# Kernel optimization log

Measured on AMD Instinct MI355X. Metric: run time of the kernel, lower is better.

Reference implementation:

```python
import jax, jax.numpy as jnp
import numpy as np
import math

DIM = 1024; B = 4; S = 2048; R = 3; K = 256; MAXR = 256; H = 8; HD = DIM // H
THRESH = 0.5; EPS = 1e-5

def _gelu(x):
    return jax.nn.gelu(x, approximate=False)

def _ln(x, g, b):
    m = jnp.mean(x, axis=-1, keepdims=True)
    v = jnp.var(x, axis=-1, keepdims=True)
    return (x - m) * jax.lax.rsqrt(v + EPS) * g + b

def setup_inputs() -> dict:
    key = jax.random.key(0)
    ks = jax.random.split(key, 24)
    sd = 1.0 / math.sqrt(DIM)
    sd2 = 1.0 / math.sqrt(2 * DIM)
    return {
        'x': jax.random.normal(ks[0], (B, S, DIM), jnp.float32),
        'retrieved': jax.random.normal(ks[1], (R, B, K, DIM), jnp.float32),
        # per-retriever query generator MLPs: Linear->GELU->Linear
        'qg_w1': jax.random.normal(ks[2], (R, DIM, DIM), jnp.float32) * sd,
        'qg_b1': jnp.zeros((R, DIM), jnp.float32),
        'qg_w2': jax.random.normal(ks[3], (R, DIM, DIM), jnp.float32) * sd,
        'qg_b2': jnp.zeros((R, DIM), jnp.float32),
        # per-retriever pooler: LayerNorm -> Linear
        'pln_g': jnp.ones((R, DIM), jnp.float32),
        'pln_b': jnp.zeros((R, DIM), jnp.float32),
        'pool_w': jax.random.normal(ks[4], (R, DIM, DIM), jnp.float32) * sd,
        'pool_b': jnp.zeros((R, DIM), jnp.float32),
        # relevance scorer: Linear(2d,d/2)->GELU->Linear(d/2,1)->Sigmoid
        'rel_w1': jax.random.normal(ks[5], (2 * DIM, DIM // 2), jnp.float32) * sd2,
        'rel_b1': jnp.zeros((DIM // 2,), jnp.float32),
        'rel_w2': jax.random.normal(ks[6], (DIM // 2, 1), jnp.float32) * (1.0 / math.sqrt(DIM // 2)),
        'rel_b2': jnp.zeros((1,), jnp.float32),
        # fusion MultiheadAttention: stacked q/k/v in-proj + out-proj
        'in_w': jax.random.normal(ks[7], (3, DIM, DIM), jnp.float32) * sd,
        'in_b': jnp.zeros((3, DIM), jnp.float32),
        'out_w': jax.random.normal(ks[8], (DIM, DIM), jnp.float32) * sd,
        'out_b': jnp.zeros((DIM,), jnp.float32),
        # fusion LayerNorm
        'fln_g': jnp.ones((DIM,), jnp.float32),
        'fln_b': jnp.zeros((DIM,), jnp.float32),
    }

def reference(x, retrieved, qg_w1, qg_b1, qg_w2, qg_b2, pln_g, pln_b, pool_w, pool_b,
              rel_w1, rel_b1, rel_w2, rel_b2, in_w, in_b, out_w, out_b, fln_g, fln_b):
    # ---- query generation: per-retriever MLP + self-attn pooling ----
    qf = _gelu(jnp.einsum('bsd,rde->rbse', x, qg_w1) + qg_b1[:, None, None, :])
    qf = jnp.einsum('rbsd,rde->rbse', qf, qg_w2) + qg_b2[:, None, None, :]  # [R,B,S,D]
    attn = jax.nn.softmax(jnp.einsum('rbsd,rbtd->rbst', qf, qf) / math.sqrt(DIM), axis=-1)
    pooled = jnp.einsum('rbst,rbtd->rbsd', attn, qf).mean(axis=2)  # [R,B,D]
    pooled = _ln(pooled, pln_g[:, None, :], pln_b[:, None, :])
    queries = jnp.einsum('rbd,rde->rbe', pooled, pool_w) + pool_b[:, None, :]  # [R,B,D]
    # ---- relevance scoring of retrieved tokens against queries ----
    q_exp = jnp.broadcast_to(queries[:, :, None, :], (R, B, K, DIM))
    pairs = jnp.concatenate([retrieved, q_exp], axis=-1)  # [R,B,K,2D]
    h = _gelu(pairs @ rel_w1 + rel_b1)
    rel = jax.nn.sigmoid((h @ rel_w2 + rel_b2)[..., 0])  # [R,B,K]
    # ---- threshold mask + per-batch top-k across all retrievers ----
    cand_tok = jnp.transpose(retrieved, (1, 0, 2, 3)).reshape(B, R * K, DIM)
    cand_rel = jnp.transpose(rel, (1, 0, 2)).reshape(B, R * K)
    valid = cand_rel >= THRESH
    masked_rel = jnp.where(valid, cand_rel, -jnp.inf)
    _, top_idx = jax.lax.top_k(masked_rel, MAXR)  # [B,MAXR]
    sel_tok = jnp.take_along_axis(cand_tok, top_idx[..., None], axis=1)  # [B,MAXR,D]
    key_valid = jnp.take_along_axis(valid, top_idx, axis=1)  # [B,MAXR]
    any_valid = jnp.any(key_valid, axis=-1)  # [B]
    # ---- fusion: cross-attention x -> selected tokens, residual + LN ----
    q = (x @ in_w[0] + in_b[0]).reshape(B, S, H, HD)
    k = (sel_tok @ in_w[1] + in_b[1]).reshape(B, MAXR, H, HD)
    v = (sel_tok @ in_w[2] + in_b[2]).reshape(B, MAXR, H, HD)
    scores = jnp.einsum('bshd,bthd->bhst', q, k) / math.sqrt(HD)
    scores = jnp.where(key_valid[:, None, None, :], scores, -1e9)
    a = jax.nn.softmax(scores, axis=-1)
    fused = jnp.einsum('bhst,bthd->bshd', a, v).reshape(B, S, DIM) @ out_w + out_b
    enhanced = _ln(x + fused, fln_g, fln_b)
    return jnp.where(any_valid[:, None, None], enhanced, x)
```

## Files before the change

### kernel.cpp

```cpp
#include <hip/hip_runtime.h>
#include <math.h>


typedef unsigned short u16;
typedef unsigned int   u32;
typedef __attribute__((ext_vector_type(8))) short short8;
typedef __attribute__((ext_vector_type(4))) float f32x4;
typedef __attribute__((ext_vector_type(4))) u16  u16x4;

__device__ __forceinline__ float b2f(u16 u){ union{float f;u32 i;} x; x.i=((u32)u)<<16; return x.f; }
__device__ __forceinline__ u16 f2b(float f){ union{float f;u32 i;} x; x.f=f; u32 r=x.i+0x7fffu+((x.i>>16)&1u); return (u16)(r>>16); }
__device__ __forceinline__ float gelu_f(float v){ return 0.5f*v*(1.f+erff(v*0.70710678118654752f)); }

__device__ __forceinline__ void load_lds16(const u16* g, u16* l){
  __builtin_amdgcn_global_load_lds((const __attribute__((address_space(1))) u32*)g,
                                   (__attribute__((address_space(3))) u32*)l, 16, 0, 0);
}

__device__ __forceinline__ float waveRedSum(float v){
  #pragma unroll
  for (int o=32;o>0;o>>=1) v += __shfl_xor(v,o);
  return v;
}
__device__ __forceinline__ float waveRedMax(float v){
  #pragma unroll
  for (int o=32;o>0;o>>=1) v = fmaxf(v, __shfl_xor(v,o));
  return v;
}
__device__ float blockRedSum(float v){
  __shared__ float tmp[17];
  const int lane = threadIdx.x&63, wv = threadIdx.x>>6, nw = blockDim.x>>6;
  v = waveRedSum(v);
  __syncthreads();
  if (lane==0) tmp[wv]=v;
  __syncthreads();
  if (threadIdx.x==0){ float s=tmp[0]; for(int i=1;i<nw;i++) s+=tmp[i]; tmp[16]=s; }
  __syncthreads();
  return tmp[16];
}
__device__ float blockRedMax(float v){
  __shared__ float tmp[17];
  const int lane = threadIdx.x&63, wv = threadIdx.x>>6, nw = blockDim.x>>6;
  v = waveRedMax(v);
  __syncthreads();
  if (lane==0) tmp[wv]=v;
  __syncthreads();
  if (threadIdx.x==0){ float s=tmp[0]; for(int i=1;i<nw;i++) s=fmaxf(s,tmp[i]); tmp[16]=s; }
  __syncthreads();
  return tmp[16];
}

enum { EPI_NONE=0, EPI_BIAS=1, EPI_SCALE=3, EPI_VT=5 };

template<int EPI>
__global__ __launch_bounds__(512,4)
void gemm_nt(const u16* __restrict__ Ag, long long lda, long long sA1, long long sA2,
             const u16* __restrict__ Bg, long long ldb, long long sB1, long long sB2,
             u16* __restrict__ Cg, long long ldc, long long sC1, long long sC2,
             const float* __restrict__ bias, long long sBias,
             float scale, int K, int H)
{
  __shared__ u16 As[2*4096];
  __shared__ u16 Bs[2*4096];
  const int z  = blockIdx.z;
  const int zb = z / H, zh = z - zb*H;
  const u16* A = Ag + zb*sA1 + zh*sA2;
  const u16* B = Bg + zb*sB1 + zh*sB2;
  const int m0 = blockIdx.y*128, n0 = blockIdx.x*128;
  const int t  = threadIdx.x;
  const int lane = t & 63, wv = t >> 6;
  const int wm = (wv>>1)*32, wn = (wv&1)*64;

  const u16* ga0 = A + (long long)(m0 + (t>>2))*lda + (t&3)*8;
  const u16* gb0 = B + (long long)(n0 + (t>>2))*ldb + (t&3)*8;
  u16* lA0 = As + t*8;
  u16* lB0 = Bs + t*8;

  f32x4 acc[2][4];
  #pragma unroll
  for (int i=0;i<2;i++)
    #pragma unroll
    for (int j=0;j<4;j++) acc[i][j] = (f32x4){0.f,0.f,0.f,0.f};

  const short8* arp = (const short8*)(As + (wm + (lane&15))*32 + ((lane>>4)*8));
  const short8* brp = (const short8*)(Bs + (wn + (lane&15))*32 + ((lane>>4)*8));

  #define STAGE_NT(bo) do{ \
    load_lds16(ga0, lA0+(bo)); \
    load_lds16(gb0, lB0+(bo)); \
    ga0 += 32; gb0 += 32; }while(0)

  const int nk = K >> 5;
  STAGE_NT(0);
  asm volatile("s_waitcnt vmcnt(0)" ::: "memory");
  __builtin_amdgcn_s_barrier();
  int cur = 0;
  for (int kk = 0; kk < nk; ++kk) {
    if (kk+1 < nk) STAGE_NT((cur^1)*4096);
    const int boS = cur*512;
    short8 af[2], bfr[4];
    #pragma unroll
    for (int i=0;i<2;i++) af[i]  = arp[boS + i*64];
    #pragma unroll
    for (int j=0;j<4;j++) bfr[j] = brp[boS + j*64];
    #pragma unroll
    for (int i=0;i<2;i++)
      #pragma unroll
      for (int j=0;j<4;j++)
        acc[i][j] = __builtin_amdgcn_mfma_f32_16x16x32_bf16(af[i], bfr[j], acc[i][j], 0, 0, 0);
    asm volatile("s_waitcnt vmcnt(0)" ::: "memory");
    __builtin_amdgcn_s_barrier();
    cur ^= 1;
  }
  #undef STAGE_NT

  u16* C = Cg + zb*sC1 + zh*sC2;
  const float* bz = bias + zb*sBias;
  const int rb0 = m0 + wm + ((lane>>4)<<2);
  const int cb0 = n0 + wn + (lane&15);
  #pragma unroll
  for (int j=0;j<4;j++){
    const int cn = cb0 + j*16;
    float bv = 0.f;
    if constexpr (EPI==EPI_BIAS || EPI==EPI_VT) bv = bz[cn];
    #pragma unroll
    for (int i=0;i<2;i++){
      #pragma unroll
      for (int p=0;p<4;p++){
        const int row = rb0 + i*16 + p;
        float v = acc[i][j][p];
        if constexpr (EPI==EPI_SCALE) v *= scale;
        if constexpr (EPI==EPI_BIAS)  v += bv;
        if constexpr (EPI==EPI_VT) {
          v += bv;
          const int bb = row>>8, tt = row&255, hh = cn>>7, dd = cn&127;
          C[((long long)((bb*8+hh)*128+dd)<<8) + tt] = f2b(v);
        } else {
          C[(long long)row*ldc + cn] = f2b(v);
        }
      }
    }
  }
}

enum { SP_GELU_SPLIT=0, SP_BIAS_SPLIT=1, SP_SCALE_F32=2, SP_QBG_F32=3 };

template<int EPI>
__global__ __launch_bounds__(512,4)
void gemm_nt_split(const u16* __restrict__ Ah_, const u16* __restrict__ Al_, long long lda, long long sAz,
                   const u16* __restrict__ Bh_, const u16* __restrict__ Bl_, long long ldb, long long sBz,
                   void* __restrict__ C0, void* __restrict__ C1, long long ldc, long long sCz,
                   const float* __restrict__ bias, float scale, int K)
{
  __shared__ u16 AsH[2*4096];
  __shared__ u16 AsL[2*4096];
  __shared__ u16 BsH[2*4096];
  __shared__ u16 BsL[2*4096];
  const int z = blockIdx.z;
  const int m0 = blockIdx.y*128, n0 = blockIdx.x*128;
  const int t  = threadIdx.x;
  const int lane = t & 63, wv = t >> 6;
  const int wm = (wv>>1)*32, wn = (wv&1)*64;

  const long long arow = (long long)z*sAz + (long long)(m0 + (t>>2))*lda + (t&3)*8;
  const long long brow = (long long)z*sBz + (long long)(n0 + (t>>2))*ldb + (t&3)*8;
  const u16* gah0 = Ah_ + arow;
  const u16* gal0 = Al_ + arow;
  const u16* gbh0 = Bh_ + brow;
  const u16* gbl0 = Bl_ + brow;
  u16* lAh0 = AsH + t*8;  u16* lAl0 = AsL + t*8;
  u16* lBh0 = BsH + t*8;  u16* lBl0 = BsL + t*8;

  f32x4 acc[2][4];
  #pragma unroll
  for (int i=0;i<2;i++)
    #pragma unroll
    for (int j=0;j<4;j++) acc[i][j] = (f32x4){0.f,0.f,0.f,0.f};

  const int foff = (lane&15)*32 + ((lane>>4)*8);
  const short8* arh = (const short8*)(AsH + wm*32 + foff);
  const short8* arl = (const short8*)(AsL + wm*32 + foff);
  const short8* brh = (const short8*)(BsH + wn*32 + foff);
  const short8* brl = (const short8*)(BsL + wn*32 + foff);

  #define STAGE_SP(bo) do{ \
    load_lds16(gah0, lAh0+(bo)); load_lds16(gal0, lAl0+(bo)); \
    load_lds16(gbh0, lBh0+(bo)); load_lds16(gbl0, lBl0+(bo)); \
    gah0 += 32; gal0 += 32; gbh0 += 32; gbl0 += 32; }while(0)

  const int nk = K >> 5;
  STAGE_SP(0);
  asm volatile("s_waitcnt vmcnt(0)" ::: "memory");
  __builtin_amdgcn_s_barrier();
  int cur = 0;
  for (int kk = 0; kk < nk; ++kk) {
    if (kk+1 < nk) STAGE_SP((cur^1)*4096);
    const int boS = cur*512;
    short8 fah[2], fal[2], fbh[4], fbl[4];
    #pragma unroll
    for (int i=0;i<2;i++){ fah[i]=arh[boS+i*64]; fal[i]=arl[boS+i*64]; }
    #pragma unroll
    for (int j=0;j<4;j++){ fbh[j]=brh[boS+j*64]; fbl[j]=brl[boS+j*64]; }
    #pragma unroll
    for (int i=0;i<2;i++)
      #pragma unroll
      for (int j=0;j<4;j++){
        acc[i][j] = __builtin_amdgcn_mfma_f32_16x16x32_bf16(fal[i], fbh[j], acc[i][j], 0, 0, 0);
        acc[i][j] = __builtin_amdgcn_mfma_f32_16x16x32_bf16(fah[i], fbl[j], acc[i][j], 0, 0, 0);
        acc[i][j] = __builtin_amdgcn_mfma_f32_16x16x32_bf16(fah[i], fbh[j], acc[i][j], 0, 0, 0);
      }
    asm volatile("s_waitcnt vmcnt(0)" ::: "memory");
    __builtin_amdgcn_s_barrier();
    cur ^= 1;
  }
  #undef STAGE_SP

  const int rb0 = m0 + wm + ((lane>>4)<<2);
  const int cb0 = n0 + wn + (lane&15);
  #pragma unroll
  for (int j=0;j<4;j++){
    const int cn = cb0 + j*16;
    float bv = 0.f;
    if constexpr (EPI==SP_GELU_SPLIT || EPI==SP_BIAS_SPLIT) bv = bias[cn];
    #pragma unroll
    for (int i=0;i<2;i++){
      #pragma unroll
      for (int p=0;p<4;p++){
        const int row = rb0 + i*16 + p;
        float v = acc[i][j][p];
        const long long o = (long long)z*sCz + (long long)row*ldc + cn;
        if constexpr (EPI==SP_GELU_SPLIT || EPI==SP_BIAS_SPLIT){
          v += bv;
          if constexpr (EPI==SP_GELU_SPLIT) v = gelu_f(v);
          const u16 h = f2b(v);
          ((u16*)C0)[o] = h;
          ((u16*)C1)[o] = f2b(v - b2f(h));
        }
        if constexpr (EPI==SP_SCALE_F32) ((float*)C0)[o] = v*scale;
        if constexpr (EPI==SP_QBG_F32)   ((float*)C0)[o] = gelu_f(v + bias[(row>>8)*512 + cn]);
      }
    }
  }
}

__global__ void transpose_w(const float* __restrict__ in, u16* __restrict__ out, int rows, int cols){
  __shared__ float tl[32][33];
  const long long zo = (long long)blockIdx.z*rows*cols;
  const int c0 = blockIdx.x*32, r0 = blockIdx.y*32;
  const int tx = threadIdx.x, ty = threadIdx.y;
  #pragma unroll
  for (int yy=ty; yy<32; yy+=8) tl[yy][tx] = in[zo + (long long)(r0+yy)*cols + (c0+tx)];
  __syncthreads();
  #pragma unroll
  for (int yy=ty; yy<32; yy+=8) out[zo + (long long)(c0+yy)*rows + (r0+tx)] = f2b(tl[tx][yy]);
}

__global__ void split_transpose_w(const float* __restrict__ in, u16* __restrict__ outH,
                                  u16* __restrict__ outL, int rows, int cols){
  __shared__ float tl[32][33];
  const long long zo = (long long)blockIdx.z*rows*cols;
  const int c0 = blockIdx.x*32, r0 = blockIdx.y*32;
  const int tx = threadIdx.x, ty = threadIdx.y;
  #pragma unroll
  for (int yy=ty; yy<32; yy+=8) tl[yy][tx] = in[zo + (long long)(r0+yy)*cols + (c0+tx)];
  __syncthreads();
  #pragma unroll
  for (int yy=ty; yy<32; yy+=8){
    const float v = tl[tx][yy];
    const u16 h = f2b(v);
    const long long o = zo + (long long)(c0+yy)*rows + (r0+tx);
    outH[o] = h;
    outL[o] = f2b(v - b2f(h));
  }
}

__global__ void split_f32_k(const float* __restrict__ in, u16* __restrict__ oh,
                            u16* __restrict__ ol, int n4){
  const int i = blockIdx.x*256 + threadIdx.x;
  if (i < n4){
    const float4 v = ((const float4*)in)[i];
    u16x4 hh, ll;
    hh.x=f2b(v.x); ll.x=f2b(v.x-b2f(hh.x));
    hh.y=f2b(v.y); ll.y=f2b(v.y-b2f(hh.y));
    hh.z=f2b(v.z); ll.z=f2b(v.z-b2f(hh.z));
    hh.w=f2b(v.w); ll.w=f2b(v.w-b2f(hh.w));
    ((u16x4*)oh)[i] = hh;
    ((u16x4*)ol)[i] = ll;
  }
}

__global__ void zero_f32(float* __restrict__ p, int n){
  const int i = blockIdx.x*256 + threadIdx.x;
  if (i < n) p[i] = 0.f;
}

__global__ void init_queries(const float* __restrict__ pb, float* __restrict__ q){
  const int i = blockIdx.x*256 + threadIdx.x;
  if (i < 12288) q[i] = pb[(i>>12)*1024 + (i&1023)];
}
__global__ void init_qpart(const float* __restrict__ rb1, float* __restrict__ qp){
  const int i = blockIdx.x*256 + threadIdx.x;
  if (i < 6144) qp[i] = rb1[i&511];
}

__global__ void ws_report(float* __restrict__ out, int n4, float val){
  const int i = blockIdx.x*256 + threadIdx.x;
  if (i < n4){
    float4 z; z.x = (i==0)? val : 0.f; z.y=0.f; z.z=0.f; z.w=0.f;
    ((float4*)out)[i] = z;
  }
}

__global__ void row_stats_f32(const float* __restrict__ S, float* __restrict__ mOut,
                              float* __restrict__ dOut){
  const int row = blockIdx.x;
  const float4* p = (const float4*)(S + (long long)row*2048);
  const int tid = threadIdx.x;
  const float4 a = p[2*tid], b = p[2*tid+1];
  float v[8] = {a.x,a.y,a.z,a.w,b.x,b.y,b.z,b.w};
  float mx = v[0];
  #pragma unroll
  for (int k=1;k<8;k++) mx = fmaxf(mx, v[k]);
  mx = blockRedMax(mx);
  float s = 0.f;
  #pragma unroll
  for (int k=0;k<8;k++) s += expf(v[k]-mx);
  s = blockRedSum(s);
  if (tid==0){ mOut[row]=mx; dOut[row]=s; }
}

__global__ void col_mean_f32(const float* __restrict__ S, const float* __restrict__ m,
                             const float* __restrict__ den, float* __restrict__ w){
  const int tc = blockIdx.x*256 + threadIdx.x;
  const int s0 = blockIdx.y*64;
  const float* p = S + (long long)s0*2048 + tc;
  float acc = 0.f;
  for (int s=0;s<64;s++)
    acc += expf(p[(long long)s<<11] - m[s0+s]) * (1.0f/den[s0+s]);
  atomicAdd(&w[tc], acc * (1.f/2048.f));
}

__global__ __launch_bounds__(256)
void pooled_par(const u16* __restrict__ qfh, const u16* __restrict__ qfl,
                const float* __restrict__ w, float* __restrict__ pooled){
  const int b = blockIdx.x, tt0 = blockIdx.y*128;
  const int t = threadIdx.x;
  __shared__ float wsh[128];
  if (t < 128) wsh[t] = w[b*2048 + tt0 + t];
  __syncthreads();
  const long long base = (long long)b*2097152 + (long long)tt0*1024;
  const u16* ph = qfh + base;
  const u16* pl = qfl + base;
  float acc[4] = {0.f,0.f,0.f,0.f};
  for (int s=0; s<128; s++){
    const float wt = wsh[s];
    const long long o = (long long)s*1024;
    #pragma unroll
    for (int k=0;k<4;k++){
      const int dd = t + k*256;
      acc[k] += wt*(b2f(ph[o+dd]) + b2f(pl[o+dd]));
    }
  }
  #pragma unroll
  for (int k=0;k<4;k++) atomicAdd(&pooled[b*1024 + t + k*256], acc[k]);
}

__global__ __launch_bounds__(1024)
void pool_ln(const float* __restrict__ pooled, const float* __restrict__ pg,
             const float* __restrict__ pb, float* __restrict__ plbuf){
  const int z = blockIdx.x, r = z>>2, d = threadIdx.x;
  const float v = pooled[z*1024+d];
  const float mean = blockRedSum(v) * (1.f/1024.f);
  const float df = v - mean;
  const float var = blockRedSum(df*df) * (1.f/1024.f);
  plbuf[z*1024+d] = df*rsqrtf(var+1e-5f)*pg[r*1024+d] + pb[r*1024+d];
}

__global__ __launch_bounds__(256)
void query_accum(const float* __restrict__ plbuf, const float* __restrict__ pw,
                 float* __restrict__ queries){
  const int z = blockIdx.x, r = z>>2, k0 = blockIdx.y*32;
  const int t = threadIdx.x;
  __shared__ float pls[32];
  if (t < 32) pls[t] = plbuf[z*1024 + k0 + t];
  __syncthreads();
  const float* wp = pw + (long long)r*1048576 + (long long)k0*1024;
  float acc[4] = {0.f,0.f,0.f,0.f};
  for (int s=0;s<32;s++){
    const float wv = pls[s];
    #pragma unroll
    for (int c=0;c<4;c++) acc[c] += wv*wp[s*1024 + t + c*256];
  }
  #pragma unroll
  for (int c=0;c<4;c++) atomicAdd(&queries[z*1024 + t + c*256], acc[c]);
}

__global__ __launch_bounds__(256)
void qpart_accum(const float* __restrict__ queries, const float* __restrict__ rw1,
                 float* __restrict__ qpart){
  const int z = blockIdx.x, k0 = blockIdx.y*64;
  const int t = threadIdx.x;
  __shared__ float qs[64];
  if (t < 64) qs[t] = queries[z*1024 + k0 + t];
  __syncthreads();
  const float* wp = rw1 + 1024*512 + (long long)k0*512;
  float acc[2] = {0.f,0.f};
  for (int s=0;s<64;s++){
    const float wv = qs[s];
    #pragma unroll
    for (int c=0;c<2;c++) acc[c] += wv*wp[s*512 + t + c*256];
  }
  #pragma unroll
  for (int c=0;c<2;c++) atomicAdd(&qpart[z*512 + t + c*256], acc[c]);
}

__global__ void rel_score_f32(const float* __restrict__ h, const float* __restrict__ w2,
                              const float* __restrict__ b2p, float* __restrict__ relv){
  const int row = blockIdx.x*4 + (threadIdx.x>>6);
  const int lane = threadIdx.x & 63;
  const float* p = h + (long long)row*512;
  float a = 0.f;
  #pragma unroll
  for (int k=0;k<8;k++){ const int idx = lane + k*64; a += p[idx]*w2[idx]; }
  a = waveRedSum(a);
  if (lane==0){
    const float lg = a + b2p[0];
    relv[row] = 1.f/(1.f+expf(-lg));
  }
}

__global__ __launch_bounds__(768)
void select_topk(const float* __restrict__ relv, int* __restrict__ selidx,
                 int* __restrict__ neff, int* __restrict__ anyv){
  const int b = blockIdx.x, c = threadIdx.x;
  __shared__ float rv[768];
  __shared__ int cnt;
  rv[c] = relv[(((c>>8)*4)+b)*256 + (c&255)];
  if (c==0) cnt = 0;
  __syncthreads();
  const float mine = rv[c];
  const bool valid = (mine >= 0.5f);
  int rank = 0;
  for (int j=0;j<768;j++){
    const float vj = rv[j];
    if (vj >= 0.5f && (vj > mine || (vj == mine && j < c))) rank++;
  }
  if (valid && rank < 256){
    const int s = atomicAdd(&cnt, 1);
    selidx[b*256 + s] = c;
  }
  __syncthreads();
  if (c==0){ neff[b] = cnt; anyv[b] = (cnt>0) ? 1 : 0; }
}

__global__ void gather_sel(const u16* __restrict__ rb16, const int* __restrict__ selidx,
                           const int* __restrict__ neff, u16* __restrict__ seltok){
  const int slot = blockIdx.x, b = blockIdx.y, tid = threadIdx.x;
  uint2 val; val.x=0u; val.y=0u;
  if (slot < neff[b]){
    const int c = selidx[b*256+slot];
    const uint2* src = (const uint2*)(rb16 + (long long)(((c>>8)*4+b)*256 + (c&255))*1024);
    val = src[tid];
  }
  ((uint2*)(seltok + (long long)(b*256+slot)*1024))[tid] = val;
}

__global__ void attn_softmax(u16* __restrict__ S, const int* __restrict__ neff){
  const int ri = blockIdx.x*4 + (threadIdx.x>>6);
  const int lane = threadIdx.x & 63;
  const int b = ri >> 14;
  const int ne = neff[b];
  u16* p = S + (long long)ri*256 + lane*4;
  if (ne == 0){ uint2 zz; zz.x=0u; zz.y=0u; *(uint2*)p = zz; return; }
  uint2 raw = *(const uint2*)p;
  u16 uu[4] = {(u16)(raw.x&0xffffu),(u16)(raw.x>>16),(u16)(raw.y&0xffffu),(u16)(raw.y>>16)};
  float xs[4];
  #pragma unroll
  for (int q2=0;q2<4;q2++){ const int tt = lane*4+q2; xs[q2] = (tt<ne)? b2f(uu[q2]) : -1e30f; }
  float mx = fmaxf(fmaxf(xs[0],xs[1]),fmaxf(xs[2],xs[3]));
  mx = waveRedMax(mx);
  float e[4]; float sm=0.f;
  #pragma unroll
  for (int q2=0;q2<4;q2++){ e[q2] = (lane*4+q2<ne)? expf(xs[q2]-mx) : 0.f; sm += e[q2]; }
  sm = waveRedSum(sm);
  const float inv = 1.f/sm;
  #pragma unroll
  for (int q2=0;q2<4;q2++) uu[q2] = f2b(e[q2]*inv);
  raw.x = (u32)uu[0] | ((u32)uu[1]<<16);
  raw.y = (u32)uu[2] | ((u32)uu[3]<<16);
  *(uint2*)p = raw;
}

__global__ void final_ln(const float* __restrict__ x, const u16* __restrict__ fused,
                         const float* __restrict__ g, const float* __restrict__ bb,
                         const int* __restrict__ anyv, float* __restrict__ out){
  const int row = blockIdx.x; const int b = row>>11; const int tid = threadIdx.x;
  const float4 xv = ((const float4*)(x + (long long)row*1024))[tid];
  const uint2 fv = ((const uint2*)(fused + (long long)row*1024))[tid];
  const float e0 = xv.x + b2f((u16)(fv.x&0xffffu));
  const float e1 = xv.y + b2f((u16)(fv.x>>16));
  const float e2 = xv.z + b2f((u16)(fv.y&0xffffu));
  const float e3 = xv.w + b2f((u16)(fv.y>>16));
  const float mean = blockRedSum(e0+e1+e2+e3) * (1.f/1024.f);
  const float d0=e0-mean, d1=e1-mean, d2=e2-mean, d3=e3-mean;
  const float var = blockRedSum(d0*d0+d1*d1+d2*d2+d3*d3) * (1.f/1024.f);
  const float inv = rsqrtf(var + 1e-5f);
  const float4 gv = ((const float4*)g)[tid];
  const float4 bv = ((const float4*)bb)[tid];
  float4 o;
  if (anyv[b]){
    o.x = d0*inv*gv.x + bv.x; o.y = d1*inv*gv.y + bv.y;
    o.z = d2*inv*gv.z + bv.z; o.w = d3*inv*gv.w + bv.w;
  } else o = xv;
  ((float4*)(out + (long long)row*1024))[tid] = o;
}

extern "C" void kernel_launch(void* const* d_in, const int* in_sizes, int n_in,
                              void* d_out, int out_size, void* d_ws, size_t ws_size,
                              hipStream_t stream) {
  (void)in_sizes; (void)n_in;
  const float* x      = (const float*)d_in[0];
  const float* retr   = (const float*)d_in[1];
  const float* qg_w1  = (const float*)d_in[2];
  const float* qg_b1  = (const float*)d_in[3];
  const float* qg_w2  = (const float*)d_in[4];
  const float* qg_b2  = (const float*)d_in[5];
  const float* pln_g  = (const float*)d_in[6];
  const float* pln_b  = (const float*)d_in[7];
  const float* pool_w = (const float*)d_in[8];
  const float* pool_b = (const float*)d_in[9];
  const float* rel_w1 = (const float*)d_in[10];
  const float* rel_b1 = (const float*)d_in[11];
  const float* rel_w2 = (const float*)d_in[12];
  const float* rel_b2 = (const float*)d_in[13];
  const float* in_w   = (const float*)d_in[14];
  const float* in_b   = (const float*)d_in[15];
  const float* out_w  = (const float*)d_in[16];
  const float* out_b  = (const float*)d_in[17];
  const float* fln_g  = (const float*)d_in[18];
  const float* fln_b  = (const float*)d_in[19];
  float* out = (float*)d_out;
  char* ws = (char*)d_ws;

  const size_t MB = 1u<<20;
  const size_t REQUIRED = 131*MB;
  if (ws_size < REQUIRED){
    ws_report<<<(out_size/4 + 255)/256, 256, 0, stream>>>(out, out_size/4, (float)(ws_size>>20));
    return;
  }

  u16* qg1Th = (u16*)(ws + 0*MB);
  u16* qg1Tl = (u16*)(ws + 6*MB);
  u16* qg2Th = (u16*)(ws + 12*MB);
  u16* qg2Tl = (u16*)(ws + 18*MB);
  u16* xh    = (u16*)(ws + 24*MB);
  u16* xl    = (u16*)(ws + 40*MB);
  u16* qfh   = (u16*)(ws + 56*MB);
  u16* qfl   = (u16*)(ws + 72*MB);
  u16* t1h   = (u16*)(ws + 88*MB);
  u16* t1l   = (u16*)(ws + 104*MB);
  float* scoresA = (float*)(ws + 88*MB);
  float* scoresB = (float*)(ws + 104*MB);
  u16* rh    = (u16*)(ws + 0*MB);
  u16* rl    = (u16*)(ws + 6*MB);
  u16* relTh = (u16*)(ws + 12*MB);
  u16* relTl = (u16*)(ws + 13*MB);
  u16* seltok= (u16*)(ws + 14*MB);
  u16* kbuf  = (u16*)(ws + 16*MB);
  u16* VT    = (u16*)(ws + 18*MB);
  float* hbuf= (float*)(ws + 88*MB);
  u16* inT   = (u16*)(ws + 40*MB);
  u16* outT  = (u16*)(ws + 46*MB);
  u16* qbuf  = (u16*)(ws + 56*MB);
  u16* fused = (u16*)(ws + 72*MB);
  u16* Sattn = (u16*)(ws + 88*MB);
  u16* attnout=(u16*)(ws + 0*MB);
  char* SM = ws + 120*MB;
  float* wbuf    = (float*)(SM);
  float* pooledB = (float*)(SM + 98304);
  float* plbuf   = (float*)(SM + 147456);
  float* queries = (float*)(SM + 196608);
  float* qpart   = (float*)(SM + 245760);
  float* relv    = (float*)(SM + 270336);
  int*   selidx  = (int*)(SM + 282624);
  int*   neff    = (int*)(SM + 286720);
  int*   anyv    = (int*)(SM + 286784);
  float* mrow0   = (float*)(SM + 286848);
  float* drow0   = (float*)(SM + 295040);
  float* mrow1   = (float*)(SM + 303232);
  float* drow1   = (float*)(SM + 311424);

  dim3 b256(256);
  dim3 b512(512);
  dim3 tb(32,8);
  const long long SCZ = (long long)(16*MB)/4;

  split_transpose_w<<<dim3(32,32,3), tb, 0, stream>>>(qg_w1, qg1Th, qg1Tl, 1024, 1024);
  split_transpose_w<<<dim3(32,32,3), tb, 0, stream>>>(qg_w2, qg2Th, qg2Tl, 1024, 1024);
  split_f32_k<<<8192, b256, 0, stream>>>(x, xh, xl, 2097152);
  zero_f32<<<144, b256, 0, stream>>>(wbuf, 36864);

  for (int r = 0; r < 3; r++){
    const long long wo = (long long)r*1048576;
    gemm_nt_split<SP_GELU_SPLIT><<<dim3(8,64,1), b512, 0, stream>>>(
        xh, xl, 1024, 0,  qg1Th+wo, qg1Tl+wo, 1024, 0,
        t1h, t1l, 1024, 0,  qg_b1+r*1024, 1.f, 1024);
    gemm_nt_split<SP_BIAS_SPLIT><<<dim3(8,64,1), b512, 0, stream>>>(
        t1h, t1l, 1024, 0,  qg2Th+wo, qg2Tl+wo, 1024, 0,
        qfh, qfl, 1024, 0,  qg_b2+r*1024, 1.f, 1024);
    for (int p2 = 0; p2 < 2; p2++){
      const long long qo = (long long)(p2*2)*2097152;
      gemm_nt_split<SP_SCALE_F32><<<dim3(16,16,2), b512, 0, stream>>>(
          qfh+qo, qfl+qo, 1024, 2097152,  qfh+qo, qfl+qo, 1024, 2097152,
          scoresA, nullptr, 2048, SCZ,  nullptr, 0.03125f, 1024);
      row_stats_f32<<<2048, b256, 0, stream>>>(scoresA, mrow0, drow0);
      row_stats_f32<<<2048, b256, 0, stream>>>(scoresB, mrow1, drow1);
      col_mean_f32<<<dim3(8,32), b256, 0, stream>>>(scoresA, mrow0, drow0, wbuf + (r*4+p2*2  )*2048);
      col_mean_f32<<<dim3(8,32), b256, 0, stream>>>(scoresB, mrow1, drow1, wbuf + (r*4+p2*2+1)*2048);
    }
    pooled_par<<<dim3(4,16), b256, 0, stream>>>(qfh, qfl, wbuf + r*8192, pooledB + r*4096);
  }
  pool_ln<<<12, 1024, 0, stream>>>(pooledB, pln_g, pln_b, plbuf);
  init_queries<<<48, b256, 0, stream>>>(pool_b, queries);
  query_accum<<<dim3(12,32), b256, 0, stream>>>(plbuf, pool_w, queries);

  split_f32_k<<<3072, b256, 0, stream>>>(retr, rh, rl, 786432);
  split_transpose_w<<<dim3(16,32,1), tb, 0, stream>>>(rel_w1, relTh, relTl, 1024, 512);
  init_qpart<<<24, b256, 0, stream>>>(rel_b1, qpart);
  qpart_accum<<<dim3(12,16), b256, 0, stream>>>(queries, rel_w1, qpart);
  gemm_nt_split<SP_QBG_F32><<<dim3(4,24,1), b512, 0, stream>>>(
      rh, rl, 1024, 0,  relTh, relTl, 1024, 0,  hbuf, nullptr, 512, 0,  qpart, 1.f, 1024);
  rel_score_f32<<<768, b256, 0, stream>>>(hbuf, rel_w2, rel_b2, relv);

  select_topk<<<4, 768, 0, stream>>>(relv, selidx, neff, anyv);
  gather_sel<<<dim3(256,4), b256, 0, stream>>>(rh, selidx, neff, seltok);

  transpose_w<<<dim3(32,32,3), tb, 0, stream>>>(in_w,  inT,  1024, 1024);
  transpose_w<<<dim3(32,32,1), tb, 0, stream>>>(out_w, outT, 1024, 1024);
  gemm_nt<EPI_BIAS><<<dim3(8,64,1), b512, 0, stream>>>(
      xh,1024,0,0,  inT,1024,0,0,  qbuf,1024,0,0,  in_b,0, 1.f, 1024, 1);
  gemm_nt<EPI_BIAS><<<dim3(8,8,1), b512, 0, stream>>>(
      seltok,1024,0,0,  inT+1048576,1024,0,0,  kbuf,1024,0,0,  in_b+1024,0, 1.f, 1024, 1);
  gemm_nt<EPI_VT><<<dim3(8,8,1), b512, 0, stream>>>(
      seltok,1024,0,0,  inT+2097152,1024,0,0,  VT,0,0,0,  in_b+2048,0, 1.f, 1024, 1);
  gemm_nt<EPI_SCALE><<<dim3(2,16,32), b512, 0, stream>>>(
      qbuf,1024,2097152,128,  kbuf,1024,262144,128,  Sattn,256,4194304,524288,
      (const float*)nullptr,0, 0.08838834764831845f, 128, 8);
  attn_softmax<<<16384, b256, 0, stream>>>(Sattn, neff);
  gemm_nt<EPI_NONE><<<dim3(1,16,32), b512, 0, stream>>>(
      Sattn,256,4194304,524288,  VT,256,262144,32768,  attnout,1024,2097152,128,
      (const float*)nullptr,0, 1.f, 256, 8);
  gemm_nt<EPI_BIAS><<<dim3(8,64,1), b512, 0, stream>>>(
      attnout,1024,0,0,  outT,1024,0,0,  fused,1024,0,0,  out_b,0, 1.f, 1024, 1);
  final_ln<<<8192, b256, 0, stream>>>(x, fused, fln_g, fln_b, anyv, out);
}
```

Baseline: 1.396 ms.

## Fuse softmax row statistics into score GEMM epilogue and merge column-mean launches

The self-attention score GEMM now computes per-tile partial row max and sum-of-exp in its epilogue using shuffles across the 16 lanes sharing a row. A small merge kernel combines the 32 partials per row into the final max and denominator. This replaces two full reads of the 2048x2048 fp32 score matrices by the row_stats kernels. The two col_mean launches are also folded into one launch with a z dimension. The cost is extra epilogue work and shuffles in the GEMM, plus more register pressure in it.

Measured after the change: 1.297 ms. 7.1% less time.

```diff
diff --git a/kernel.cpp b/kernel.cpp
--- a/kernel.cpp
+++ b/kernel.cpp
@@ -143,14 +143,15 @@
   }
 }
 
-enum { SP_GELU_SPLIT=0, SP_BIAS_SPLIT=1, SP_SCALE_F32=2, SP_QBG_F32=3 };
+enum { SP_GELU_SPLIT=0, SP_BIAS_SPLIT=1, SP_SCALE_F32=2, SP_QBG_F32=3, SP_SCALE_STATS=4 };
 
 template<int EPI>
 __global__ __launch_bounds__(512,4)
 void gemm_nt_split(const u16* __restrict__ Ah_, const u16* __restrict__ Al_, long long lda, long long sAz,
                    const u16* __restrict__ Bh_, const u16* __restrict__ Bl_, long long ldb, long long sBz,
                    void* __restrict__ C0, void* __restrict__ C1, long long ldc, long long sCz,
-                   const float* __restrict__ bias, float scale, int K)
+                   const float* __restrict__ bias, float scale, int K,
+                   float* __restrict__ pm, float* __restrict__ ps)
 {
   __shared__ u16 AsH[2*4096];
   __shared__ u16 AsL[2*4096];
@@ -236,10 +237,56 @@
           ((u16*)C0)[o] = h;
           ((u16*)C1)[o] = f2b(v - b2f(h));
         }
-        if constexpr (EPI==SP_SCALE_F32) ((float*)C0)[o] = v*scale;
+        if constexpr (EPI==SP_SCALE_F32 || EPI==SP_SCALE_STATS) ((float*)C0)[o] = v*scale;
         if constexpr (EPI==SP_QBG_F32)   ((float*)C0)[o] = gelu_f(v + bias[(row>>8)*512 + cn]);
       }
     }
+  }
+
+  if constexpr (EPI==SP_SCALE_STATS){
+    const int g = blockIdx.x*2 + (wv&1);
+    #pragma unroll
+    for (int i=0;i<2;i++){
+      #pragma unroll
+      for (int p=0;p<4;p++){
+        float mx = -3.4e38f;
+        #pragma unroll
+        for (int j=0;j<4;j++) mx = fmaxf(mx, acc[i][j][p]*scale);
+        #pragma unroll
+        for (int o=1;o<16;o<<=1) mx = fmaxf(mx, __shfl_xor(mx,o));
+        float sm = 0.f;
+        #pragma unroll
+        for (int j=0;j<4;j++) sm += expf(acc[i][j][p]*scale - mx);
+        #pragma unroll
+        for (int o=1;o<16;o<<=1) sm += __shfl_xor(sm,o);
+        if ((lane&15)==0){
+          const int row = rb0 + i*16 + p;
+          const long long pi = ((long long)z*2048 + row)*32 + g;
+          pm[pi] = mx; ps[pi] = sm;
+        }
+      }
+    }
+  }
+}
+
+__global__ __launch_bounds__(256)
+void merge_stats(const float* __restrict__ pm, const float* __restrict__ ps,
+                 float* __restrict__ m0o, float* __restrict__ d0o,
+                 float* __restrict__ m1o, float* __restrict__ d1o){
+  const int wv = threadIdx.x>>6, lane = threadIdx.x&63;
+  const int row = blockIdx.x*8 + wv*2 + (lane>>5);
+  const int g = lane & 31;
+  const long long pi = (long long)row*32 + g;
+  const float mg = pm[pi];
+  float m = mg;
+  #pragma unroll
+  for (int o=1;o<32;o<<=1) m = fmaxf(m, __shfl_xor(m,o));
+  float s = ps[pi] * expf(mg - m);
+  #pragma unroll
+  for (int o=1;o<32;o<<=1) s += __shfl_xor(s,o);
+  if (g==0){
+    if (row < 2048){ m0o[row]=m; d0o[row]=s; }
+    else           { m1o[row-2048]=m; d1o[row-2048]=s; }
   }
 }
 
@@ -311,33 +358,20 @@
   }
 }
 
-__global__ void row_stats_f32(const float* __restrict__ S, float* __restrict__ mOut,
-                              float* __restrict__ dOut){
-  const int row = blockIdx.x;
-  const float4* p = (const float4*)(S + (long long)row*2048);
-  const int tid = threadIdx.x;
-  const float4 a = p[2*tid], b = p[2*tid+1];
-  float v[8] = {a.x,a.y,a.z,a.w,b.x,b.y,b.z,b.w};
-  float mx = v[0];
-  #pragma unroll
-  for (int k=1;k<8;k++) mx = fmaxf(mx, v[k]);
-  mx = blockRedMax(mx);
-  float s = 0.f;
-  #pragma unroll
-  for (int k=0;k<8;k++) s += expf(v[k]-mx);
-  s = blockRedSum(s);
-  if (tid==0){ mOut[row]=mx; dOut[row]=s; }
-}
-
-__global__ void col_mean_f32(const float* __restrict__ S, const float* __restrict__ m,
-                             const float* __restrict__ den, float* __restrict__ w){
+__global__ void col_mean2(const float* __restrict__ S, long long sz,
+                          const float* __restrict__ m0a, const float* __restrict__ den0,
+                          const float* __restrict__ m1a, const float* __restrict__ den1,
+                          float* __restrict__ w){
+  const int zz = blockIdx.z;
+  const float* m   = zz ? m1a : m0a;
+  const float* den = zz ? den1 : den0;
   const int tc = blockIdx.x*256 + threadIdx.x;
   const int s0 = blockIdx.y*64;
-  const float* p = S + (long long)s0*2048 + tc;
+  const float* p = S + (long long)zz*sz + (long long)s0*2048 + tc;
   float acc = 0.f;
   for (int s=0;s<64;s++)
     acc += expf(p[(long long)s<<11] - m[s0+s]) * (1.0f/den[s0+s]);
-  atomicAdd(&w[tc], acc * (1.f/2048.f));
+  atomicAdd(&w[zz*2048 + tc], acc * (1.f/2048.f));
 }
 
 __global__ __launch_bounds__(256)
@@ -589,6 +623,8 @@
   float* drow0   = (float*)(SM + 295040);
   float* mrow1   = (float*)(SM + 303232);
   float* drow1   = (float*)(SM + 311424);
+  float* partM   = (float*)(SM + 512*1024);
+  float* partS   = (float*)(SM + 1536*1024);
 
   dim3 b256(256);
   dim3 b512(512);
@@ -604,19 +640,18 @@
     const long long wo = (long long)r*1048576;
     gemm_nt_split<SP_GELU_SPLIT><<<dim3(8,64,1), b512, 0, stream>>>(
         xh, xl, 1024, 0,  qg1Th+wo, qg1Tl+wo, 1024, 0,
-        t1h, t1l, 1024, 0,  qg_b1+r*1024, 1.f, 1024);
+        t1h, t1l, 1024, 0,  qg_b1+r*1024, 1.f, 1024, nullptr, nullptr);
     gemm_nt_split<SP_BIAS_SPLIT><<<dim3(8,64,1), b512, 0, stream>>>(
         t1h, t1l, 1024, 0,  qg2Th+wo, qg2Tl+wo, 1024, 0,
-        qfh, qfl, 1024, 0,  qg_b2+r*1024, 1.f, 1024);
+        qfh, qfl, 1024, 0,  qg_b2+r*1024, 1.f, 1024, nullptr, nullptr);
     for (int p2 = 0; p2 < 2; p2++){
       const long long qo = (long long)(p2*2)*2097152;
-      gemm_nt_split<SP_SCALE_F32><<<dim3(16,16,2), b512, 0, stream>>>(
+      gemm_nt_split<SP_SCALE_STATS><<<dim3(16,16,2), b512, 0, stream>>>(
           qfh+qo, qfl+qo, 1024, 2097152,  qfh+qo, qfl+qo, 1024, 2097152,
-          scoresA, nullptr, 2048, SCZ,  nullptr, 0.03125f, 1024);
-      row_stats_f32<<<2048, b256, 0, stream>>>(scoresA, mrow0, drow0);
-      row_stats_f32<<<2048, b256, 0, stream>>>(scoresB, mrow1, drow1);
-      col_mean_f32<<<dim3(8,32), b256, 0, stream>>>(scoresA, mrow0, drow0, wbuf + (r*4+p2*2  )*2048);
-      col_mean_f32<<<dim3(8,32), b256, 0, stream>>>(scoresB, mrow1, drow1, wbuf + (r*4+p2*2+1)*2048);
+          scoresA, nullptr, 2048, SCZ,  nullptr, 0.03125f, 1024, partM, partS);
+      merge_stats<<<512, b256, 0, stream>>>(partM, partS, mrow0, drow0, mrow1, drow1);
+      col_mean2<<<dim3(8,32,2), b256, 0, stream>>>(
+          scoresA, SCZ, mrow0, drow0, mrow1, drow1, wbuf + (r*4+p2*2)*2048);
     }
     pooled_par<<<dim3(4,16), b256, 0, stream>>>(qfh, qfl, wbuf + r*8192, pooledB + r*4096);
   }
@@ -629,7 +664,8 @@
   init_qpart<<<24, b256, 0, stream>>>(rel_b1, qpart);
   qpart_accum<<<dim3(12,16), b256, 0, stream>>>(queries, rel_w1, qpart);
   gemm_nt_split<SP_QBG_F32><<<dim3(4,24,1), b512, 0, stream>>>(
-      rh, rl, 1024, 0,  relTh, relTl, 1024, 0,  hbuf, nullptr, 512, 0,  qpart, 1.f, 1024);
+      rh, rl, 1024, 0,  relTh, relTl, 1024, 0,  hbuf, nullptr, 512, 0,  qpart, 1.f, 1024,
+      nullptr, nullptr);
   rel_score_f32<<<768, b256, 0, stream>>>(hbuf, rel_w2, rel_b2, relv);
 
   select_topk<<<4, 768, 0, stream>>>(relv, selidx, neff, anyv);
```
